# Kernel optimization log

Hardware: AMD Instinct MI355X
Metric: run time of the kernel (lower is better)

Reference implementation:

```python
import jax, jax.numpy as jnp
import numpy as np

B, S, D = 4, 2048, 1024
H = 16
HD = D // H

def setup_inputs() -> dict:
    key = jax.random.key(0)
    ks = jax.random.split(key, 5)
    x = jax.random.normal(ks[0], (B, S, D), dtype=jnp.float32)
    # PyTorch Linear: y = x @ W.T + b; store W in torch layout [out, in]
    w_qkv = jax.random.normal(ks[1], (3 * D, D), dtype=jnp.float32) * (1.0 / np.sqrt(D))
    b_qkv = jax.random.normal(ks[2], (3 * D,), dtype=jnp.float32) * 0.01
    w_out = jax.random.normal(ks[3], (D, D), dtype=jnp.float32) * (1.0 / np.sqrt(D))
    b_out = jax.random.normal(ks[4], (D,), dtype=jnp.float32) * 0.01
    return {"x": x, "w_qkv": w_qkv, "b_qkv": b_qkv, "w_out": w_out, "b_out": b_out}

def reference(x, w_qkv, b_qkv, w_out, b_out):
    b, s, d = x.shape
    qkv = x @ w_qkv.T + b_qkv                      # [B,S,3D]
    q, k, v = jnp.split(qkv, 3, axis=2)
    # [B,S,D] -> [B,H,S,HD]
    q = q.reshape(b, s, H, HD).transpose(0, 2, 1, 3)
    k = k.reshape(b, s, H, HD).transpose(0, 2, 1, 3)
    v = v.reshape(b, s, H, HD).transpose(0, 2, 1, 3)
    att = jnp.einsum('bhqd,bhkd->bhqk', q, k) / np.sqrt(HD)
    causal = jnp.tril(jnp.ones((s, s), dtype=bool))
    att = jnp.where(causal[None, None], att, -jnp.inf)
    att = jax.nn.softmax(att, axis=-1)
    y = jnp.einsum('bhqk,bhkd->bhqd', att, v)      # [B,H,S,HD]
    y = y.transpose(0, 2, 1, 3).reshape(b, s, d)
    return y @ w_out.T + b_out
```

## Files before the change

kernel.cpp:

```cpp
#include <hip/hip_runtime.h>
#include <hip/hip_bf16.h>

#define DEV __device__ __forceinline__

typedef __attribute__((ext_vector_type(8))) short bf16x8;
typedef __attribute__((ext_vector_type(4))) float f32x4;

#define BB 4
#define SS 2048
#define DD 1024
#define HH 16
#define HDD 64
#define MM (BB * SS)
#define NT (SS / 64)
#define NQT (SS / 128)

DEV short f2bf(float f) {
  unsigned u = __builtin_bit_cast(unsigned, f);
  u = u + 0x7fffu + ((u >> 16) & 1u);
  return (short)(u >> 16);
}

DEV float fexp2(float x) {
  float r;
  asm("v_exp_f32 %0, %1" : "=v"(r) : "v"(x));
  return r;
}
DEV float frcp(float x) {
  float r;
  asm("v_rcp_f32 %0, %1" : "=v"(r) : "v"(x));
  return r;
}
DEV unsigned cvtpk(float a, float b) {
  unsigned r;
  asm("v_cvt_pk_bf16_f32 %0, %1, %2" : "=v"(r) : "v"(a), "v"(b));
  return r;
}

DEV void gload_lds16(const void* g, void* l) {
  __builtin_amdgcn_global_load_lds((const __attribute__((address_space(1))) void*)g,
                                   (__attribute__((address_space(3))) void*)l, 16, 0, 0);
}

DEV int2 xcd_swizzle() {
  const int nx = gridDim.x;
  const int nwg = nx * gridDim.y;
  const int o = blockIdx.y * nx + blockIdx.x;
  const int wid = (o & 7) * (nwg >> 3) + (o >> 3);
  int2 r; r.x = wid % nx; r.y = wid / nx;
  return r;
}

DEV void cast_range(const float* __restrict__ in, unsigned long long* __restrict__ out,
                    int n4, int start, int stride) {
  for (int i = start; i < n4; i += stride) {
    const float4 f = ((const float4*)in)[i];
    unsigned long long a = (unsigned long long)(unsigned short)f2bf(f.x)
        | ((unsigned long long)(unsigned short)f2bf(f.y) << 16)
        | ((unsigned long long)(unsigned short)f2bf(f.z) << 32)
        | ((unsigned long long)(unsigned short)f2bf(f.w) << 48);
    out[i] = a;
  }
}

__global__ __launch_bounds__(256)
void cast3_f32_bf16(const float* __restrict__ x, unsigned long long* __restrict__ ox, int nx4,
                    const float* __restrict__ wq, unsigned long long* __restrict__ owq, int nwq4,
                    const float* __restrict__ wo, unsigned long long* __restrict__ owo, int nwo4) {
  const int start = blockIdx.x * 256 + threadIdx.x;
  const int stride = gridDim.x * 256;
  cast_range(x, ox, nx4, start, stride);
  cast_range(wq, owq, nwq4, start, stride);
  cast_range(wo, owo, nwo4, start, stride);
}

template<int EPI>
__global__ __launch_bounds__(256)
void gemm_bt(const short* __restrict__ A, const short* __restrict__ Bw,
             const float* __restrict__ bias,
             short* __restrict__ qo, short* __restrict__ ko, short* __restrict__ vo,
             float* __restrict__ co,
             int M, int N, int K) {
  __shared__ short sA[2][128 * 64];
  __shared__ short sB[2][128 * 64];
  const int lane = threadIdx.x & 63;
  const int wv = threadIdx.x >> 6;
  const int wm = wv >> 1, wn = wv & 1;
  const int2 sw = xcd_swizzle();
  const int m0 = sw.y * 128;
  const int n0 = sw.x * 128;
  const int lr = lane & 15;
  const int lg = lane >> 4;
  const int lm = lr & 7;

  int srow[4], soff[4], doff[4];
#pragma unroll
  for (int i = 0; i < 4; ++i) {
    const int e = (i * 4 + wv) * 64 + lane;
    const int row = e >> 3;
    srow[i] = row;
    soff[i] = ((e & 7) ^ (row & 7)) * 8;
    doff[i] = e * 8;
  }

  f32x4 acc[4][4] = {};
  const int nkt = K >> 6;

#pragma unroll
  for (int i = 0; i < 4; ++i) {
    gload_lds16(A  + (size_t)(m0 + srow[i]) * K + soff[i], &sA[0][doff[i]]);
    gload_lds16(Bw + (size_t)(n0 + srow[i]) * K + soff[i], &sB[0][doff[i]]);
  }

  int cur = 0;
  for (int kt = 0; kt < nkt; ++kt) {
    __syncthreads();
    if (kt + 1 < nkt) {
      const int k1 = (kt + 1) << 6;
#pragma unroll
      for (int i = 0; i < 4; ++i) {
        gload_lds16(A  + (size_t)(m0 + srow[i]) * K + k1 + soff[i], &sA[cur ^ 1][doff[i]]);
        gload_lds16(Bw + (size_t)(n0 + srow[i]) * K + k1 + soff[i], &sB[cur ^ 1][doff[i]]);
      }
    }
#pragma unroll
    for (int ks = 0; ks < 2; ++ks) {
      const int slot = (((ks << 2) + lg) ^ lm) * 8;
      bf16x8 af[4], bf_[4];
#pragma unroll
      for (int i = 0; i < 4; ++i) {
        af[i]  = *(const bf16x8*)&sA[cur][(wm * 64 + i * 16 + lr) * 64 + slot];
        bf_[i] = *(const bf16x8*)&sB[cur][(wn * 64 + i * 16 + lr) * 64 + slot];
      }
#pragma unroll
      for (int i = 0; i < 4; ++i)
#pragma unroll
        for (int j = 0; j < 4; ++j)
          acc[i][j] = __builtin_amdgcn_mfma_f32_16x16x32_bf16(af[i], bf_[j], acc[i][j], 0, 0, 0);
    }
    cur ^= 1;
  }

#pragma unroll
  for (int i = 0; i < 4; ++i) {
#pragma unroll
    for (int j = 0; j < 4; ++j) {
#pragma unroll
      for (int r = 0; r < 4; ++r) {
        const int row = m0 + wm * 64 + i * 16 + lg * 4 + r;
        const int col = n0 + wn * 64 + j * 16 + lr;
        float v = acc[i][j][r] + bias[col];
        if (EPI == 0) {
          const int part = col >> 10, oo = col & 1023;
          const int h = oo >> 6, d = oo & 63;
          const int bb = row >> 11, s = row & 2047;
          if (part == 0)
            qo[(((size_t)bb * HH + h) * SS + s) * HDD + d] = f2bf(v * 0.18033688f);
          else if (part == 1)
            ko[(((size_t)bb * HH + h) * SS + s) * HDD + d] = f2bf(v);
          else {
            const int q = (s >> 2) & 15;
            const int tau = (q & 8) | ((q & 3) << 1) | ((q >> 2) & 1);
            vo[(((size_t)bb * HH + h) * HDD + d) * SS + (s & ~63) + (tau << 2) + (s & 3)] = f2bf(v);
          }
        } else {
          co[(size_t)row * N + col] = v;
        }
      }
    }
  }
}

__global__ __launch_bounds__(256)
void attn_fwd(const short* __restrict__ Q, const short* __restrict__ K,
              const short* __restrict__ V, short* __restrict__ Y) {
  __shared__ short sK[2][64 * 64];
  __shared__ short sV[2][64 * 64];
  const int2 sw = xcd_swizzle();
  const int bh = sw.y;
  const int bx = sw.x;
  const int tid = threadIdx.x, lane = tid & 63, w = tid >> 6;
  const size_t bqk = (size_t)bh * (SS * HDD);
  const size_t bv  = (size_t)bh * (HDD * SS);
  const int b = bh >> 4, h = bh & 15;
  const int lr = lane & 15;
  const int lg = lane >> 4;
  const int lm = lr & 7;

  const int e0 = w * 64 + lane;
  const int e1 = 256 + e0;
  const int r0 = e0 >> 3, s0 = ((e0 & 7) ^ (r0 & 7)) * 8;
  const int r1 = e1 >> 3, s1 = ((e1 & 7) ^ (r1 & 7)) * 8;

  for (int qsel = 0; qsel < 2; ++qsel) {
    const int qt = qsel ? (NQT - 1 - bx) : bx;
    const int q0 = qt * 128;
    const int nkv = 2 * qt + 2;

    __syncthreads();

    {
      const short* gK = K + bqk;
      const short* gV = V + bv;
      gload_lds16(gK + (size_t)r0 * HDD + s0, &sK[0][e0 * 8]);
      gload_lds16(gV + (size_t)r0 * SS + s0, &sV[0][e0 * 8]);
      gload_lds16(gK + (size_t)r1 * HDD + s1, &sK[0][e1 * 8]);
      gload_lds16(gV + (size_t)r1 * SS + s1, &sV[0][e1 * 8]);
    }

    const int qbase = q0 + w * 32;
    bf16x8 qf[2][2];
#pragma unroll
    for (int g = 0; g < 2; ++g)
#pragma unroll
      for (int ks = 0; ks < 2; ++ks)
        qf[g][ks] = *(const bf16x8*)&Q[bqk + (size_t)(qbase + g * 16 + lr) * HDD + ks * 32 + lg * 8];

    f32x4 accO[2][4] = {};
    float m_[2] = {-1e30f, -1e30f}, l_[2] = {0.f, 0.f};

    int cur = 0;
    for (int kt = 0; kt < nkv; ++kt) {
      const int kc0 = kt * 64;
      __syncthreads();
      if (kt < nkv - 1) {
        const short* gK = K + bqk + (size_t)(kc0 + 64) * 64;
        const short* gV = V + bv + kc0 + 64;
        gload_lds16(gK + (size_t)r0 * HDD + s0, &sK[cur ^ 1][e0 * 8]);
        gload_lds16(gV + (size_t)r0 * SS + s0, &sV[cur ^ 1][e0 * 8]);
        gload_lds16(gK + (size_t)r1 * HDD + s1, &sK[cur ^ 1][e1 * 8]);
        gload_lds16(gV + (size_t)r1 * SS + s1, &sV[cur ^ 1][e1 * 8]);
      }

      f32x4 st[2][4] = {};
#pragma unroll
      for (int ks = 0; ks < 2; ++ks) {
#pragma unroll
        for (int nf = 0; nf < 4; ++nf) {
          const int row = nf * 16 + lr;
          const bf16x8 kf = *(const bf16x8*)&sK[cur][row * 64 + (((ks << 2) + lg) ^ lm) * 8];
          st[0][nf] = __builtin_amdgcn_mfma_f32_16x16x32_bf16(kf, qf[0][ks], st[0][nf], 0, 0, 0);
          st[1][nf] = __builtin_amdgcn_mfma_f32_16x16x32_bf16(kf, qf[1][ks], st[1][nf], 0, 0, 0);
        }
      }
      if (kt >= nkv - 2) {
#pragma unroll
        for (int g = 0; g < 2; ++g) {
          const int q = qbase + g * 16 + lr;
#pragma unroll
          for (int nf = 0; nf < 4; ++nf)
#pragma unroll
            for (int r = 0; r < 4; ++r) {
              const int k = kc0 + nf * 16 + lg * 4 + r;
              if (k > q) st[g][nf][r] = -1e30f;
            }
        }
      }

      unsigned u[2][4][2];
#pragma unroll
      for (int g = 0; g < 2; ++g) {
        float rm = -1e30f;
#pragma unroll
        for (int r = 0; r < 4; ++r)
          rm = fmaxf(rm, fmaxf(fmaxf(st[g][0][r], st[g][1][r]), fmaxf(st[g][2][r], st[g][3][r])));
        rm = fmaxf(rm, __shfl_xor(rm, 16));
        rm = fmaxf(rm, __shfl_xor(rm, 32));

        const bool need = rm > m_[g] + 11.5416f;
        if (__any(need)) {
          const float mn = fmaxf(m_[g], rm);
          const float scale = fexp2(m_[g] - mn);
          m_[g] = mn;
          l_[g] *= scale;
#pragma unroll
          for (int r = 0; r < 4; ++r) {
            const float scl = __shfl(scale, (lane & 48) + (lg << 2) + r);
#pragma unroll
            for (int df = 0; df < 4; ++df) accO[g][df][r] *= scl;
          }
        }

        float rs = 0.f;
#pragma unroll
        for (int nf = 0; nf < 4; ++nf)
#pragma unroll
          for (int r = 0; r < 4; ++r) {
            const float p = fexp2(st[g][nf][r] - m_[g]);
            st[g][nf][r] = p;
            rs += p;
          }
        rs += __shfl_xor(rs, 16);
        rs += __shfl_xor(rs, 32);
        l_[g] += rs;

#pragma unroll
        for (int nf = 0; nf < 4; ++nf) {
          u[g][nf][0] = cvtpk(st[g][nf][0], st[g][nf][1]);
          u[g][nf][1] = cvtpk(st[g][nf][2], st[g][nf][3]);
        }
      }

#pragma unroll
      for (int c = 0; c < 2; ++c) {
        int4 pw0, pw1;
        pw0.x = (int)u[0][2 * c][0]; pw0.y = (int)u[0][2 * c][1];
        pw0.z = (int)u[0][2 * c + 1][0]; pw0.w = (int)u[0][2 * c + 1][1];
        pw1.x = (int)u[1][2 * c][0]; pw1.y = (int)u[1][2 * c][1];
        pw1.z = (int)u[1][2 * c + 1][0]; pw1.w = (int)u[1][2 * c + 1][1];
        const bf16x8 pf0 = __builtin_bit_cast(bf16x8, pw0);
        const bf16x8 pf1 = __builtin_bit_cast(bf16x8, pw1);
        const int slot = (((c << 2) + lg) ^ lm) * 8;
#pragma unroll
        for (int df = 0; df < 4; ++df) {
          const bf16x8 vf = *(const bf16x8*)&sV[cur][(df * 16 + lr) * 64 + slot];
          accO[0][df] = __builtin_amdgcn_mfma_f32_16x16x32_bf16(pf0, vf, accO[0][df], 0, 0, 0);
          accO[1][df] = __builtin_amdgcn_mfma_f32_16x16x32_bf16(pf1, vf, accO[1][df], 0, 0, 0);
        }
      }
      cur ^= 1;
    }

#pragma unroll
    for (int g = 0; g < 2; ++g)
#pragma unroll
      for (int r = 0; r < 4; ++r) {
        const float lv = __shfl(l_[g], (lane & 48) + (lg << 2) + r);
        const float inv = frcp(lv);
        const int srow2 = qbase + g * 16 + lg * 4 + r;
#pragma unroll
        for (int df = 0; df < 4; ++df) {
          const int dcol = h * HDD + df * 16 + lr;
          Y[((size_t)b * SS + srow2) * DD + dcol] = f2bf(accO[g][df][r] * inv);
        }
      }
  }
}

extern "C" void kernel_launch(void* const* d_in, const int* in_sizes, int n_in,
                              void* d_out, int out_size, void* d_ws, size_t ws_size,
                              hipStream_t stream) {
  const float* x     = (const float*)d_in[0];
  const float* w_qkv = (const float*)d_in[1];
  const float* b_qkv = (const float*)d_in[2];
  const float* w_out = (const float*)d_in[3];
  const float* b_out = (const float*)d_in[4];
  float* out = (float*)d_out;

  const size_t nx = (size_t)MM * DD;
  const size_t nwq = (size_t)3 * DD * DD;
  const size_t nwo = (size_t)DD * DD;

  short* x_bf    = (short*)d_ws;
  short* wqkv_bf = x_bf + nx;
  short* wout_bf = wqkv_bf + nwq;
  short* q_ws    = wout_bf + nwo;
  short* k_ws    = q_ws + nx;
  short* v_ws    = k_ws + nx;
  short* y_ws    = v_ws + nx;

  cast3_f32_bf16<<<dim3(2048), dim3(256), 0, stream>>>(
      x, (unsigned long long*)x_bf, (int)(nx / 4),
      w_qkv, (unsigned long long*)wqkv_bf, (int)(nwq / 4),
      w_out, (unsigned long long*)wout_bf, (int)(nwo / 4));

  gemm_bt<0><<<dim3(3 * DD / 128, MM / 128), dim3(256), 0, stream>>>(
      x_bf, wqkv_bf, b_qkv, q_ws, k_ws, v_ws, nullptr, MM, 3 * DD, DD);

  attn_fwd<<<dim3(NQT / 2, BB * HH), dim3(256), 0, stream>>>(q_ws, k_ws, v_ws, y_ws);

  gemm_bt<1><<<dim3(DD / 128, MM / 128), dim3(256), 0, stream>>>(
      y_ws, wout_bf, b_out, nullptr, nullptr, nullptr, out, MM, DD, DD);
}
```

Before: 190.9 us.

## Use 8-wave 256-row GEMM tiles with split fragment loads and priority hints

Replaces the 4-wave 128x128 GEMM with a templated 8-wave (512-thread) kernel using 256xBN tiles: 256x256 for the QKV projection and 256x128 for the output projection. The larger tiles are meant to cut global and LDS traffic per MFMA and raise arithmetic intensity. The K-step is split into four phases with barriers between them, and setprio is raised around each MFMA block to interleave LDS reads with matrix math across waves. In exchange it uses more LDS (up to 128KB), more registers, extra barriers and fewer blocks, which lowers occupancy and leaves fewer tiles to balance across CUs.

```diff
diff --git a/kernel.cpp b/kernel.cpp
--- a/kernel.cpp
+++ b/kernel.cpp
@@ -12,7 +12,6 @@
 #define HH 16
 #define HDD 64
 #define MM (BB * SS)
-#define NT (SS / 64)
 #define NQT (SS / 128)
 
 DEV short f2bf(float f) {
@@ -74,81 +73,104 @@
   cast_range(wo, owo, nwo4, start, stride);
 }
 
-template<int EPI>
-__global__ __launch_bounds__(256)
-void gemm_bt(const short* __restrict__ A, const short* __restrict__ Bw,
-             const float* __restrict__ bias,
-             short* __restrict__ qo, short* __restrict__ ko, short* __restrict__ vo,
-             float* __restrict__ co,
-             int M, int N, int K) {
-  __shared__ short sA[2][128 * 64];
-  __shared__ short sB[2][128 * 64];
-  const int lane = threadIdx.x & 63;
-  const int wv = threadIdx.x >> 6;
-  const int wm = wv >> 1, wn = wv & 1;
+template<int EPI, int BN, int WGM, int WGN>
+__global__ __launch_bounds__(512)
+void gemm8(const short* __restrict__ A, const short* __restrict__ Bw,
+           const float* __restrict__ bias,
+           short* __restrict__ qo, short* __restrict__ ko, short* __restrict__ vo,
+           float* __restrict__ co,
+           int M, int N, int K) {
+  constexpr int WTM = 256 / WGM;
+  constexpr int WTN = BN / WGN;
+  constexpr int FM = WTM / 16;
+  constexpr int FN = WTN / 16;
+  constexpr int NBI = BN / 64;
+  __shared__ short sA[2][256 * 64];
+  __shared__ short sB[2][BN * 64];
+  const int tid = threadIdx.x;
+  const int lane = tid & 63;
+  const int wid = tid >> 6;
+  const int wm = wid / WGN, wn = wid % WGN;
   const int2 sw = xcd_swizzle();
-  const int m0 = sw.y * 128;
-  const int n0 = sw.x * 128;
+  const int m0 = sw.y * 256;
+  const int n0 = sw.x * BN;
   const int lr = lane & 15;
   const int lg = lane >> 4;
   const int lm = lr & 7;
 
-  int srow[4], soff[4], doff[4];
+  int arow[4], asoff[4], adoff[4];
 #pragma unroll
   for (int i = 0; i < 4; ++i) {
-    const int e = (i * 4 + wv) * 64 + lane;
+    const int e = i * 512 + tid;
     const int row = e >> 3;
-    srow[i] = row;
-    soff[i] = ((e & 7) ^ (row & 7)) * 8;
-    doff[i] = e * 8;
-  }
-
-  f32x4 acc[4][4] = {};
+    arow[i] = row; asoff[i] = ((e & 7) ^ (row & 7)) * 8; adoff[i] = e * 8;
+  }
+  int brow[NBI], bsoff[NBI], bdoff[NBI];
+#pragma unroll
+  for (int i = 0; i < NBI; ++i) {
+    const int e = i * 512 + tid;
+    const int row = e >> 3;
+    brow[i] = row; bsoff[i] = ((e & 7) ^ (row & 7)) * 8; bdoff[i] = e * 8;
+  }
+
+  f32x4 acc[FM][FN] = {};
   const int nkt = K >> 6;
 
 #pragma unroll
-  for (int i = 0; i < 4; ++i) {
-    gload_lds16(A  + (size_t)(m0 + srow[i]) * K + soff[i], &sA[0][doff[i]]);
-    gload_lds16(Bw + (size_t)(n0 + srow[i]) * K + soff[i], &sB[0][doff[i]]);
-  }
+  for (int i = 0; i < 4; ++i)
+    gload_lds16(A + (size_t)(m0 + arow[i]) * K + asoff[i], &sA[0][adoff[i]]);
+#pragma unroll
+  for (int i = 0; i < NBI; ++i)
+    gload_lds16(Bw + (size_t)(n0 + brow[i]) * K + bsoff[i], &sB[0][bdoff[i]]);
 
   int cur = 0;
   for (int kt = 0; kt < nkt; ++kt) {
-    __syncthreads();
+    asm volatile("s_waitcnt vmcnt(0)" ::: "memory");
+    __builtin_amdgcn_s_barrier();
     if (kt + 1 < nkt) {
       const int k1 = (kt + 1) << 6;
 #pragma unroll
-      for (int i = 0; i < 4; ++i) {
-        gload_lds16(A  + (size_t)(m0 + srow[i]) * K + k1 + soff[i], &sA[cur ^ 1][doff[i]]);
-        gload_lds16(Bw + (size_t)(n0 + srow[i]) * K + k1 + soff[i], &sB[cur ^ 1][doff[i]]);
-      }
-    }
-#pragma unroll
-    for (int ks = 0; ks < 2; ++ks) {
+      for (int i = 0; i < 4; ++i)
+        gload_lds16(A + (size_t)(m0 + arow[i]) * K + k1 + asoff[i], &sA[cur ^ 1][adoff[i]]);
+#pragma unroll
+      for (int i = 0; i < NBI; ++i)
+        gload_lds16(Bw + (size_t)(n0 + brow[i]) * K + k1 + bsoff[i], &sB[cur ^ 1][bdoff[i]]);
+    }
+    bf16x8 bfr[FN];
+#pragma unroll
+    for (int q = 0; q < 4; ++q) {
+      const int ks = q >> 1, hf = q & 1;
       const int slot = (((ks << 2) + lg) ^ lm) * 8;
-      bf16x8 af[4], bf_[4];
-#pragma unroll
-      for (int i = 0; i < 4; ++i) {
-        af[i]  = *(const bf16x8*)&sA[cur][(wm * 64 + i * 16 + lr) * 64 + slot];
-        bf_[i] = *(const bf16x8*)&sB[cur][(wn * 64 + i * 16 + lr) * 64 + slot];
-      }
-#pragma unroll
-      for (int i = 0; i < 4; ++i)
-#pragma unroll
-        for (int j = 0; j < 4; ++j)
-          acc[i][j] = __builtin_amdgcn_mfma_f32_16x16x32_bf16(af[i], bf_[j], acc[i][j], 0, 0, 0);
+      if (hf == 0) {
+#pragma unroll
+        for (int nf = 0; nf < FN; ++nf)
+          bfr[nf] = *(const bf16x8*)&sB[cur][(wn * WTN + nf * 16 + lr) * 64 + slot];
+      }
+      bf16x8 afr[FM / 2];
+#pragma unroll
+      for (int f = 0; f < FM / 2; ++f)
+        afr[f] = *(const bf16x8*)&sA[cur][(wm * WTM + (hf * (FM / 2) + f) * 16 + lr) * 64 + slot];
+      __builtin_amdgcn_s_setprio(1);
+#pragma unroll
+      for (int f = 0; f < FM / 2; ++f)
+#pragma unroll
+        for (int nf = 0; nf < FN; ++nf)
+          acc[hf * (FM / 2) + f][nf] =
+              __builtin_amdgcn_mfma_f32_16x16x32_bf16(afr[f], bfr[nf], acc[hf * (FM / 2) + f][nf], 0, 0, 0);
+      __builtin_amdgcn_s_setprio(0);
+      if (q < 3) __builtin_amdgcn_s_barrier();
     }
     cur ^= 1;
   }
 
 #pragma unroll
-  for (int i = 0; i < 4; ++i) {
-#pragma unroll
-    for (int j = 0; j < 4; ++j) {
+  for (int i = 0; i < FM; ++i) {
+#pragma unroll
+    for (int j = 0; j < FN; ++j) {
 #pragma unroll
       for (int r = 0; r < 4; ++r) {
-        const int row = m0 + wm * 64 + i * 16 + lg * 4 + r;
-        const int col = n0 + wn * 64 + j * 16 + lr;
+        const int row = m0 + wm * WTM + i * 16 + lg * 4 + r;
+        const int col = n0 + wn * WTN + j * 16 + lr;
         float v = acc[i][j][r] + bias[col];
         if (EPI == 0) {
           const int part = col >> 10, oo = col & 1023;
@@ -159,8 +181,8 @@
           else if (part == 1)
             ko[(((size_t)bb * HH + h) * SS + s) * HDD + d] = f2bf(v);
           else {
-            const int q = (s >> 2) & 15;
-            const int tau = (q & 8) | ((q & 3) << 1) | ((q >> 2) & 1);
+            const int q2 = (s >> 2) & 15;
+            const int tau = (q2 & 8) | ((q2 & 3) << 1) | ((q2 >> 2) & 1);
             vo[(((size_t)bb * HH + h) * HDD + d) * SS + (s & ~63) + (tau << 2) + (s & 3)] = f2bf(v);
           }
         } else {
@@ -364,11 +386,11 @@
       w_qkv, (unsigned long long*)wqkv_bf, (int)(nwq / 4),
       w_out, (unsigned long long*)wout_bf, (int)(nwo / 4));
 
-  gemm_bt<0><<<dim3(3 * DD / 128, MM / 128), dim3(256), 0, stream>>>(
+  gemm8<0, 256, 2, 4><<<dim3(3 * DD / 256, MM / 256), dim3(512), 0, stream>>>(
       x_bf, wqkv_bf, b_qkv, q_ws, k_ws, v_ws, nullptr, MM, 3 * DD, DD);
 
   attn_fwd<<<dim3(NQT / 2, BB * HH), dim3(256), 0, stream>>>(q_ws, k_ws, v_ws, y_ws);
 
-  gemm_bt<1><<<dim3(DD / 128, MM / 128), dim3(256), 0, stream>>>(
+  gemm8<1, 128, 4, 2><<<dim3(DD / 128, MM / 256), dim3(512), 0, stream>>>(
       y_ws, wout_bf, b_out, nullptr, nullptr, nullptr, out, MM, DD, DD);
 }
```

New measurement: 214.3 us. 12.3% more time.

## Triple-buffer GEMM with 256x128 tiles, 8 waves and explicit waitcnt pipelining

Applied to the files above, without the earlier changes.

Replaces the double-buffered 128x128 GEMM with a 512-thread kernel that computes 256x128 tiles and uses a three-stage LDS ring, so global loads run two K-tiles ahead. Explicit vmcnt waits, raw s_barrier, sched_barrier and setprio around the MFMA block are meant to overlap memory with compute and give matrix work priority. The larger tile raises B reuse per block. In exchange it uses 144KB of LDS and one block per CU, which halves the grid and can hurt occupancy or tail balance, especially for the smaller output projection GEMM.

```diff
diff --git a/kernel.cpp b/kernel.cpp
--- a/kernel.cpp
+++ b/kernel.cpp
@@ -12,7 +12,6 @@
 #define HH 16
 #define HDD 64
 #define MM (BB * SS)
-#define NT (SS / 64)
 #define NQT (SS / 128)
 
 DEV short f2bf(float f) {
@@ -75,70 +74,91 @@
 }
 
 template<int EPI>
-__global__ __launch_bounds__(256)
-void gemm_bt(const short* __restrict__ A, const short* __restrict__ Bw,
+__global__ __launch_bounds__(512, 1)
+void gemm_c3(const short* __restrict__ A, const short* __restrict__ Bw,
              const float* __restrict__ bias,
              short* __restrict__ qo, short* __restrict__ ko, short* __restrict__ vo,
              float* __restrict__ co,
              int M, int N, int K) {
-  __shared__ short sA[2][128 * 64];
-  __shared__ short sB[2][128 * 64];
-  const int lane = threadIdx.x & 63;
-  const int wv = threadIdx.x >> 6;
-  const int wm = wv >> 1, wn = wv & 1;
+  __shared__ short sA[3][256 * 64];
+  __shared__ short sB[3][128 * 64];
+  const int tid = threadIdx.x;
+  const int lane = tid & 63;
+  const int wid = tid >> 6;
+  const int wm = wid >> 1, wn = wid & 1;
   const int2 sw = xcd_swizzle();
-  const int m0 = sw.y * 128;
-  const int n0 = sw.x * 128;
-  const int lr = lane & 15;
-  const int lg = lane >> 4;
+  const int m0 = sw.y * 256, n0 = sw.x * 128;
+  const int lr = lane & 15, lg = lane >> 4;
   const int lm = lr & 7;
 
-  int srow[4], soff[4], doff[4];
+  int aro[4], aso[4], ado[4];
 #pragma unroll
   for (int i = 0; i < 4; ++i) {
-    const int e = (i * 4 + wv) * 64 + lane;
+    const int e = i * 512 + tid;
     const int row = e >> 3;
-    srow[i] = row;
-    soff[i] = ((e & 7) ^ (row & 7)) * 8;
-    doff[i] = e * 8;
+    aro[i] = row; aso[i] = ((e & 7) ^ (row & 7)) * 8; ado[i] = e * 8;
+  }
+  int bro[2], bso[2], bdo_[2];
+#pragma unroll
+  for (int i = 0; i < 2; ++i) {
+    const int e = i * 512 + tid;
+    const int row = e >> 3;
+    bro[i] = row; bso[i] = ((e & 7) ^ (row & 7)) * 8; bdo_[i] = e * 8;
+  }
+
+  const int nkt = K >> 6;
+
+#pragma unroll
+  for (int p = 0; p < 2; ++p) {
+    const int kk = p << 6;
+#pragma unroll
+    for (int i = 0; i < 4; ++i)
+      gload_lds16(A + (size_t)(m0 + aro[i]) * K + kk + aso[i], &sA[p][ado[i]]);
+#pragma unroll
+    for (int i = 0; i < 2; ++i)
+      gload_lds16(Bw + (size_t)(n0 + bro[i]) * K + kk + bso[i], &sB[p][bdo_[i]]);
   }
 
   f32x4 acc[4][4] = {};
-  const int nkt = K >> 6;
-
-#pragma unroll
-  for (int i = 0; i < 4; ++i) {
-    gload_lds16(A  + (size_t)(m0 + srow[i]) * K + soff[i], &sA[0][doff[i]]);
-    gload_lds16(Bw + (size_t)(n0 + srow[i]) * K + soff[i], &sB[0][doff[i]]);
-  }
-
-  int cur = 0;
-  for (int kt = 0; kt < nkt; ++kt) {
-    __syncthreads();
-    if (kt + 1 < nkt) {
-      const int k1 = (kt + 1) << 6;
-#pragma unroll
-      for (int i = 0; i < 4; ++i) {
-        gload_lds16(A  + (size_t)(m0 + srow[i]) * K + k1 + soff[i], &sA[cur ^ 1][doff[i]]);
-        gload_lds16(Bw + (size_t)(n0 + srow[i]) * K + k1 + soff[i], &sB[cur ^ 1][doff[i]]);
-      }
-    }
+  int buf = 0;
+  for (int t = 0; t < nkt; ++t) {
+    if (t + 1 < nkt) asm volatile("s_waitcnt vmcnt(6)" ::: "memory");
+    else             asm volatile("s_waitcnt vmcnt(0)" ::: "memory");
+    __builtin_amdgcn_s_barrier();
+    __builtin_amdgcn_sched_barrier(0);
+
+    if (t + 2 < nkt) {
+      const int kk = (t + 2) << 6;
+      const int pb = (buf + 2 >= 3) ? buf - 1 : buf + 2;
+#pragma unroll
+      for (int i = 0; i < 4; ++i)
+        gload_lds16(A + (size_t)(m0 + aro[i]) * K + kk + aso[i], &sA[pb][ado[i]]);
+#pragma unroll
+      for (int i = 0; i < 2; ++i)
+        gload_lds16(Bw + (size_t)(n0 + bro[i]) * K + kk + bso[i], &sB[pb][bdo_[i]]);
+    }
+
 #pragma unroll
     for (int ks = 0; ks < 2; ++ks) {
       const int slot = (((ks << 2) + lg) ^ lm) * 8;
-      bf16x8 af[4], bf_[4];
-#pragma unroll
-      for (int i = 0; i < 4; ++i) {
-        af[i]  = *(const bf16x8*)&sA[cur][(wm * 64 + i * 16 + lr) * 64 + slot];
-        bf_[i] = *(const bf16x8*)&sB[cur][(wn * 64 + i * 16 + lr) * 64 + slot];
-      }
+      bf16x8 afr[4], bfr[4];
 #pragma unroll
       for (int i = 0; i < 4; ++i)
+        afr[i] = *(const bf16x8*)&sA[buf][(wm * 64 + i * 16 + lr) * 64 + slot];
+#pragma unroll
+      for (int j = 0; j < 4; ++j)
+        bfr[j] = *(const bf16x8*)&sB[buf][(wn * 64 + j * 16 + lr) * 64 + slot];
+      asm volatile("s_waitcnt lgkmcnt(0)" ::: "memory");
+      __builtin_amdgcn_sched_barrier(0);
+      __builtin_amdgcn_s_setprio(1);
+#pragma unroll
+      for (int i = 0; i < 4; ++i)
 #pragma unroll
         for (int j = 0; j < 4; ++j)
-          acc[i][j] = __builtin_amdgcn_mfma_f32_16x16x32_bf16(af[i], bf_[j], acc[i][j], 0, 0, 0);
-    }
-    cur ^= 1;
+          acc[i][j] = __builtin_amdgcn_mfma_f32_16x16x32_bf16(afr[i], bfr[j], acc[i][j], 0, 0, 0);
+      __builtin_amdgcn_s_setprio(0);
+    }
+    buf = (buf + 1 >= 3) ? 0 : buf + 1;
   }
 
 #pragma unroll
@@ -159,8 +179,8 @@
           else if (part == 1)
             ko[(((size_t)bb * HH + h) * SS + s) * HDD + d] = f2bf(v);
           else {
-            const int q = (s >> 2) & 15;
-            const int tau = (q & 8) | ((q & 3) << 1) | ((q >> 2) & 1);
+            const int q2 = (s >> 2) & 15;
+            const int tau = (q2 & 8) | ((q2 & 3) << 1) | ((q2 >> 2) & 1);
             vo[(((size_t)bb * HH + h) * HDD + d) * SS + (s & ~63) + (tau << 2) + (s & 3)] = f2bf(v);
           }
         } else {
@@ -364,11 +384,11 @@
       w_qkv, (unsigned long long*)wqkv_bf, (int)(nwq / 4),
       w_out, (unsigned long long*)wout_bf, (int)(nwo / 4));
 
-  gemm_bt<0><<<dim3(3 * DD / 128, MM / 128), dim3(256), 0, stream>>>(
+  gemm_c3<0><<<dim3(3 * DD / 128, MM / 256), dim3(512), 0, stream>>>(
       x_bf, wqkv_bf, b_qkv, q_ws, k_ws, v_ws, nullptr, MM, 3 * DD, DD);
 
   attn_fwd<<<dim3(NQT / 2, BB * HH), dim3(256), 0, stream>>>(q_ws, k_ws, v_ws, y_ws);
 
-  gemm_bt<1><<<dim3(DD / 128, MM / 128), dim3(256), 0, stream>>>(
+  gemm_c3<1><<<dim3(DD / 128, MM / 256), dim3(512), 0, stream>>>(
       y_ws, wout_bf, b_out, nullptr, nullptr, nullptr, out, MM, DD, DD);
 }
```

After: 206.6 us. +8.2%, slower.

## Replace double-buffered GEMM LDS pipeline with single-buffer load-sync-compute loop

Applied to the files above, without the earlier changes.

The GEMM kernel drops its two-stage shared-memory double buffer. Each K step now loads the A and B tiles into a single buffer, synchronises, then computes, so LDS use is halved. The intent is to let more blocks fit per compute unit, and that higher occupancy is meant to hide latency instead of software prefetch. In exchange, global-to-LDS loads no longer overlap with MFMA work inside a block, and there is an extra barrier per iteration.

```diff
diff --git a/kernel.cpp b/kernel.cpp
--- a/kernel.cpp
+++ b/kernel.cpp
@@ -12,7 +12,6 @@
 #define HH 16
 #define HDD 64
 #define MM (BB * SS)
-#define NT (SS / 64)
 #define NQT (SS / 128)
 
 DEV short f2bf(float f) {
@@ -81,8 +80,8 @@
              short* __restrict__ qo, short* __restrict__ ko, short* __restrict__ vo,
              float* __restrict__ co,
              int M, int N, int K) {
-  __shared__ short sA[2][128 * 64];
-  __shared__ short sB[2][128 * 64];
+  __shared__ short sA[128 * 64];
+  __shared__ short sB[128 * 64];
   const int lane = threadIdx.x & 63;
   const int wv = threadIdx.x >> 6;
   const int wm = wv >> 1, wn = wv & 1;
@@ -96,7 +95,7 @@
   int srow[4], soff[4], doff[4];
 #pragma unroll
   for (int i = 0; i < 4; ++i) {
-    const int e = (i * 4 + wv) * 64 + lane;
+    const int e = i * 256 + threadIdx.x;
     const int row = e >> 3;
     srow[i] = row;
     soff[i] = ((e & 7) ^ (row & 7)) * 8;
@@ -105,32 +104,23 @@
 
   f32x4 acc[4][4] = {};
   const int nkt = K >> 6;
-
-#pragma unroll
-  for (int i = 0; i < 4; ++i) {
-    gload_lds16(A  + (size_t)(m0 + srow[i]) * K + soff[i], &sA[0][doff[i]]);
-    gload_lds16(Bw + (size_t)(n0 + srow[i]) * K + soff[i], &sB[0][doff[i]]);
-  }
-
-  int cur = 0;
   for (int kt = 0; kt < nkt; ++kt) {
+    const int k0 = kt << 6;
+    if (kt) __syncthreads();
+#pragma unroll
+    for (int i = 0; i < 4; ++i) {
+      gload_lds16(A  + (size_t)(m0 + srow[i]) * K + k0 + soff[i], &sA[doff[i]]);
+      gload_lds16(Bw + (size_t)(n0 + srow[i]) * K + k0 + soff[i], &sB[doff[i]]);
+    }
     __syncthreads();
-    if (kt + 1 < nkt) {
-      const int k1 = (kt + 1) << 6;
-#pragma unroll
-      for (int i = 0; i < 4; ++i) {
-        gload_lds16(A  + (size_t)(m0 + srow[i]) * K + k1 + soff[i], &sA[cur ^ 1][doff[i]]);
-        gload_lds16(Bw + (size_t)(n0 + srow[i]) * K + k1 + soff[i], &sB[cur ^ 1][doff[i]]);
-      }
-    }
 #pragma unroll
     for (int ks = 0; ks < 2; ++ks) {
       const int slot = (((ks << 2) + lg) ^ lm) * 8;
       bf16x8 af[4], bf_[4];
 #pragma unroll
       for (int i = 0; i < 4; ++i) {
-        af[i]  = *(const bf16x8*)&sA[cur][(wm * 64 + i * 16 + lr) * 64 + slot];
-        bf_[i] = *(const bf16x8*)&sB[cur][(wn * 64 + i * 16 + lr) * 64 + slot];
+        af[i]  = *(const bf16x8*)&sA[(wm * 64 + i * 16 + lr) * 64 + slot];
+        bf_[i] = *(const bf16x8*)&sB[(wn * 64 + i * 16 + lr) * 64 + slot];
       }
 #pragma unroll
       for (int i = 0; i < 4; ++i)
@@ -138,7 +128,6 @@
         for (int j = 0; j < 4; ++j)
           acc[i][j] = __builtin_amdgcn_mfma_f32_16x16x32_bf16(af[i], bf_[j], acc[i][j], 0, 0, 0);
     }
-    cur ^= 1;
   }
 
 #pragma unroll
@@ -159,8 +148,8 @@
           else if (part == 1)
             ko[(((size_t)bb * HH + h) * SS + s) * HDD + d] = f2bf(v);
           else {
-            const int q = (s >> 2) & 15;
-            const int tau = (q & 8) | ((q & 3) << 1) | ((q >> 2) & 1);
+            const int q2 = (s >> 2) & 15;
+            const int tau = (q2 & 8) | ((q2 & 3) << 1) | ((q2 >> 2) & 1);
             vo[(((size_t)bb * HH + h) * HDD + d) * SS + (s & ~63) + (tau << 2) + (s & 3)] = f2bf(v);
           }
         } else {
```

Measured after the change: 190.4 us. About the same (-0.3%).
